# Optimization experiments

Hardware: AMD Instinct MI355X
Metric: run time of the kernel (lower is better)

## Reference

```python
import jax, jax.numpy as jnp
import numpy as np

IN_CH = 64
OUT_CH = 32
SCALE = 2
BLOCK = SCALE ** 3  # 8
N = 400000   # input sparse voxels (lines in pair_fwd)
M = 200000   # output sparse voxels


def setup_inputs() -> dict:
    key = jax.random.key(0)
    k1, k2, k3 = jax.random.split(key, 3)
    x_features = jax.random.normal(k1, (N, IN_CH), dtype=jnp.float32)
    # flat ParameterList: weights[i*BLOCK + j] is the (in_channels,) weight for
    # output channel i, kernel position j
    weights = jax.random.normal(k2, (BLOCK * OUT_CH, IN_CH), dtype=jnp.float32)
    # spconv pair_fwd: [kernel_volume, num_lines], -1 marks invalid mapping
    pair_fwd = jax.random.randint(k3, (BLOCK, N), -1, M)
    return {"x_features": x_features, "weights": weights,
            "pair_fwd": pair_fwd, "num_out": M}


def reference(x_features, weights, pair_fwd, num_out):
    block, n = pair_fwd.shape
    out_ch = weights.shape[0] // block
    # W[o, j, c] == weights_list[o*block + j]
    W = weights.reshape(out_ch, block, -1)
    # sequential VoxelShuffle then .view(-1) per block is identity on each
    # voxel's in_channels feature vector, so:
    # vals[j, n, o] = dot(W[o, j, :], x_features[n, :])
    vals = jnp.einsum('nc,ojc->jno', x_features, W)  # [block, N, out_ch]
    idx = pair_fwd.reshape(-1)                       # [block*N]
    # route invalid (-1) entries to a dummy trailing row
    safe = jnp.where(idx >= 0, idx, num_out)
    buf = jnp.zeros((num_out + 1, out_ch), dtype=vals.dtype)
    # original uses assignment (set) semantics into out_features
    buf = buf.at[safe].set(vals.reshape(block * n, out_ch))
    return buf[:num_out]
```

## Files before the change

kernel.cpp:

```cpp
#include <hip/hip_runtime.h>

#define IN_CH  64
#define OUT_CH 32
#define BLOCK  8
#define ROWS   8


__global__ void k_prep(int4* __restrict__ argmax4, int n4, int* __restrict__ cur) {
    int i = blockIdx.x * 256 + threadIdx.x;
    if (i < 16) cur[i] = 0;
    if (i < n4) argmax4[i] = make_int4(-1, -1, -1, -1);
}

__global__ void k_scatter_range(const int* __restrict__ pair, int* __restrict__ argmax,
                                int N, int jhi, int jlo, int flip) {
    int n = blockIdx.x * 256 + threadIdx.x;
    if (n >= N) return;
    if (flip) n = N - 1 - n;
    for (int j = jhi; j >= jlo; --j) {
        int t = j * N + n;
        int m = pair[t];
        if (m >= 0 && argmax[m] < t)
            atomicMax(&argmax[m], t);
    }
}

__global__ void k_fill(const int* __restrict__ argmax, int* __restrict__ cur,
                       int* __restrict__ bm, int* __restrict__ bn, int M, int N) {
    __shared__ int h9[9];
    __shared__ int b9[9];
    if (threadIdx.x < 9) h9[threadIdx.x] = 0;
    __syncthreads();
    int m = blockIdx.x * 256 + threadIdx.x;
    int j = 9, n = 0, lo = 0;
    if (m < M) {
        int t = argmax[m];
        if (t >= 0) { j = (int)((unsigned)t / (unsigned)N); n = t - j * N; }
        else j = 8;
        lo = atomicAdd(&h9[j], 1);
    }
    __syncthreads();
    if (threadIdx.x < 9 && h9[threadIdx.x] > 0)
        b9[threadIdx.x] = atomicAdd(&cur[threadIdx.x], h9[threadIdx.x]);
    __syncthreads();
    if (m < M) {
        int pos = j * M + b9[j] + lo;
        bm[pos] = m;
        bn[pos] = n;
    }
}

__global__ __launch_bounds__(512, 4) void k_compute(
        const float* __restrict__ x, const float* __restrict__ w,
        const int* __restrict__ cnt, const int* __restrict__ bm,
        const int* __restrict__ bn, float* __restrict__ out, int M, int N) {
    __shared__ __align__(16) float Xl[8][2][ROWS * 64];

    const int lane = threadIdx.x & 63;
    const int o    = lane & 31;
    const int hh   = lane >> 5;
    const int wv   = threadIdx.x >> 6;

    int T = blockIdx.x * 8 + wv;
    int j = 0, nrows = 0;
    for (; j < 9; ++j) {
        int c  = cnt[j];
        int nt = (c + 63) >> 6;
        if (T < nt) { nrows = min(64, c - T * 64); break; }
        T -= nt;
    }
    if (j >= 9) return;
    int base = j * M + T * 64;

    int jw = (j < 8) ? j : 0;
    float4 wreg[8];
#pragma unroll
    for (int k = 0; k < 8; ++k)
        wreg[k] = *(const float4*)&w[(o * BLOCK + jw) * IN_CH + hh * 32 + k * 4];

    int mm = 0, nn = 0;
    if (lane < nrows) { mm = bm[base + lane]; nn = bn[base + lane]; }

    int ntiles = (nrows + ROWS - 1) / ROWS;
    float ld[ROWS];

#pragma unroll
    for (int r = 0; r < ROWS; ++r) {
        int n = __builtin_amdgcn_readlane(nn, r);
        ld[r] = x[(size_t)n * IN_CH + lane];
    }

    for (int tile = 0; tile < ntiles; ++tile) {
        float* buf = &Xl[wv][tile & 1][0];
#pragma unroll
        for (int r = 0; r < ROWS; ++r)
            buf[r * 64 + lane] = ld[r];

        if (tile + 1 < ntiles) {
            int nb = (tile + 1) * ROWS;
#pragma unroll
            for (int r = 0; r < ROWS; ++r) {
                int n = __builtin_amdgcn_readlane(nn, nb + r);
                ld[r] = x[(size_t)n * IN_CH + lane];
            }
        }

        asm volatile("s_waitcnt lgkmcnt(0)" ::: "memory");

#pragma unroll
        for (int r = 0; r < ROWS; r += 2) {
            int grow = tile * ROWS + r;
            float s01[2];
#pragma unroll
            for (int p = 0; p < 2; ++p) {
                const float4* xp = (const float4*)(buf + (r + p) * 64) + hh * 8;
                float ax = 0.f, ay = 0.f, az = 0.f, aw = 0.f;
#pragma unroll
                for (int k = 0; k < 8; ++k) {
                    float4 xv = xp[k];
                    ax = fmaf(wreg[k].x, xv.x, ax);
                    ay = fmaf(wreg[k].y, xv.y, ay);
                    az = fmaf(wreg[k].z, xv.z, az);
                    aw = fmaf(wreg[k].w, xv.w, aw);
                }
                float s = (ax + ay) + (az + aw);
                s += __shfl_xor(s, 32);
                s01[p] = s;
            }
            float sv   = hh ? s01[1] : s01[0];
            int   m0   = __builtin_amdgcn_readlane(mm, grow);
            int   m1   = __builtin_amdgcn_readlane(mm, grow + 1);
            int   mrow = hh ? m1 : m0;
            if (j == 8) sv = 0.f;
            int orow = grow + hh;
            if (orow < nrows)
                out[(size_t)mrow * OUT_CH + o] = sv;
        }
    }
}

extern "C" void kernel_launch(void* const* d_in, const int* in_sizes, int n_in,
                              void* d_out, int out_size, void* d_ws, size_t ws_size,
                              hipStream_t stream) {
    const float* x    = (const float*)d_in[0];
    const float* w    = (const float*)d_in[1];
    const int*   pair = (const int*)d_in[2];
    int N = in_sizes[0] / IN_CH;
    int M = out_size / OUT_CH;

    char* ws     = (char*)d_ws;
    int*  cur    = (int*)ws;
    int*  argmax = (int*)(ws + 256);
    int*  bm     = (int*)(ws + 256 + (size_t)M * 4);
    int*  bn     = (int*)(ws + 256 + (size_t)M * 4 + (size_t)9 * M * 4);

    int n4 = M / 4;
    k_prep<<<(n4 + 255) / 256, 256, 0, stream>>>((int4*)argmax, n4, cur);

    int gN = (N + 255) / 256;
    k_scatter_range<<<gN, 256, 0, stream>>>(pair, argmax, N, 7, 7, 1);
    k_scatter_range<<<gN, 256, 0, stream>>>(pair, argmax, N, 6, 0, 0);

    k_fill<<<(M + 255) / 256, 256, 0, stream>>>(argmax, cur, bm, bn, M, N);

    int maxtiles = (M + 63) / 64 + 8;
    int blocks   = (maxtiles + 7) / 8;
    k_compute<<<blocks, 512, 0, stream>>>(x, w, cur, bm, bn, (float*)d_out, M, N);
}
```

Measured before the change: 99.79 us.

## Compute gathered rows with bf16 MFMA instead of fp32 FMA via LDS

Replaces the per-lane fp32 dot-product loop, which staged rows through shared memory, with bf16 MFMA 16x16x32 instructions. Activations and weights are converted to bf16 in registers, and x rows are gathered straight from global memory without the LDS double buffer. Blocks shrink to 256 threads. This cuts ALU and LDS traffic but lowers precision to bf16 inputs, which risks tolerance failures.

```diff
diff --git a/kernel.cpp b/kernel.cpp
--- a/kernel.cpp
+++ b/kernel.cpp
@@ -3,7 +3,9 @@
 #define IN_CH  64
 #define OUT_CH 32
 #define BLOCK  8
-#define ROWS   8
+
+using short8 = __attribute__((ext_vector_type(8))) short;
+using f32x4v = __attribute__((ext_vector_type(4))) float;
 
 
 __global__ void k_prep(int4* __restrict__ argmax4, int n4, int* __restrict__ cur) {
@@ -50,18 +52,31 @@
     }
 }
 
-__global__ __launch_bounds__(512, 4) void k_compute(
+__device__ __forceinline__ unsigned cvt_pk_bf16(float lo, float hi) {
+    unsigned r;
+    asm("v_cvt_pk_bf16_f32 %0, %1, %2" : "=v"(r) : "v"(lo), "v"(hi));
+    return r;
+}
+
+__device__ __forceinline__ short8 pack8(float4 a, float4 b) {
+    union { unsigned u[4]; short8 s; } p;
+    p.u[0] = cvt_pk_bf16(a.x, a.y);
+    p.u[1] = cvt_pk_bf16(a.z, a.w);
+    p.u[2] = cvt_pk_bf16(b.x, b.y);
+    p.u[3] = cvt_pk_bf16(b.z, b.w);
+    return p.s;
+}
+
+__global__ __launch_bounds__(256, 4) void k_compute(
         const float* __restrict__ x, const float* __restrict__ w,
         const int* __restrict__ cnt, const int* __restrict__ bm,
         const int* __restrict__ bn, float* __restrict__ out, int M, int N) {
-    __shared__ __align__(16) float Xl[8][2][ROWS * 64];
-
     const int lane = threadIdx.x & 63;
-    const int o    = lane & 31;
-    const int hh   = lane >> 5;
+    const int r16  = lane & 15;
+    const int kc   = lane >> 4;
     const int wv   = threadIdx.x >> 6;
 
-    int T = blockIdx.x * 8 + wv;
+    int T = blockIdx.x * 4 + wv;
     int j = 0, nrows = 0;
     for (; j < 9; ++j) {
         int c  = cnt[j];
@@ -71,70 +86,49 @@
     }
     if (j >= 9) return;
     int base = j * M + T * 64;
+    int jw = (j < 8) ? j : 0;
 
-    int jw = (j < 8) ? j : 0;
-    float4 wreg[8];
+    short8 bf[2][2];
 #pragma unroll
-    for (int k = 0; k < 8; ++k)
-        wreg[k] = *(const float4*)&w[(o * BLOCK + jw) * IN_CH + hh * 32 + k * 4];
-
-    int mm = 0, nn = 0;
-    if (lane < nrows) { mm = bm[base + lane]; nn = bn[base + lane]; }
-
-    int ntiles = (nrows + ROWS - 1) / ROWS;
-    float ld[ROWS];
+    for (int ot = 0; ot < 2; ++ot)
+#pragma unroll
+        for (int kk = 0; kk < 2; ++kk) {
+            const float* wp = w + ((ot * 16 + r16) * BLOCK + jw) * IN_CH + kk * 32 + kc * 8;
+            bf[ot][kk] = pack8(*(const float4*)wp, *(const float4*)(wp + 4));
+        }
 
 #pragma unroll
-    for (int r = 0; r < ROWS; ++r) {
-        int n = __builtin_amdgcn_readlane(nn, r);
-        ld[r] = x[(size_t)n * IN_CH + lane];
-    }
+    for (int st = 0; st < 4; ++st) {
+        if (st * 16 >= nrows) break;
+        int lrow = st * 16 + r16;
+        int n    = bn[base + ((lrow < nrows) ? lrow : 0)];
+        const float* xp = x + (size_t)n * IN_CH + kc * 8;
+        float4 x0 = *(const float4*)xp;
+        float4 x1 = *(const float4*)(xp + 4);
+        float4 x2 = *(const float4*)(xp + 32);
+        float4 x3 = *(const float4*)(xp + 36);
+        short8 a0 = pack8(x0, x1);
+        short8 a1 = pack8(x2, x3);
 
-    for (int tile = 0; tile < ntiles; ++tile) {
-        float* buf = &Xl[wv][tile & 1][0];
+        f32x4v acc0 = {0.f, 0.f, 0.f, 0.f};
+        f32x4v acc1 = {0.f, 0.f, 0.f, 0.f};
+        acc0 = __builtin_amdgcn_mfma_f32_16x16x32_bf16(a0, bf[0][0], acc0, 0, 0, 0);
+        acc0 = __builtin_amdgcn_mfma_f32_16x16x32_bf16(a1, bf[0][1], acc0, 0, 0, 0);
+        acc1 = __builtin_amdgcn_mfma_f32_16x16x32_bf16(a0, bf[1][0], acc1, 0, 0, 0);
+        acc1 = __builtin_amdgcn_mfma_f32_16x16x32_bf16(a1, bf[1][1], acc1, 0, 0, 0);
+
+        int4 m4 = *(const int4*)&bm[base + st * 16 + kc * 4];
+        int ma[4] = {m4.x, m4.y, m4.z, m4.w};
 #pragma unroll
-        for (int r = 0; r < ROWS; ++r)
-            buf[r * 64 + lane] = ld[r];
-
-        if (tile + 1 < ntiles) {
-            int nb = (tile + 1) * ROWS;
-#pragma unroll
-            for (int r = 0; r < ROWS; ++r) {
-                int n = __builtin_amdgcn_readlane(nn, nb + r);
-                ld[r] = x[(size_t)n * IN_CH + lane];
+        for (int q = 0; q < 4; ++q) {
+            int grow = st * 16 + kc * 4 + q;
+            if (grow < nrows) {
+                size_t ro = (size_t)ma[q] * OUT_CH;
+                float v0 = (j == 8) ? 0.f : acc0[q];
+                float v1 = (j == 8) ? 0.f : acc1[q];
+                out[ro + r16]      = v0;
+                out[ro + 16 + r16] = v1;
             }
-        }
-
-        asm volatile("s_waitcnt lgkmcnt(0)" ::: "memory");
-
-#pragma unroll
-        for (int r = 0; r < ROWS; r += 2) {
-            int grow = tile * ROWS + r;
-            float s01[2];
-#pragma unroll
-            for (int p = 0; p < 2; ++p) {
-                const float4* xp = (const float4*)(buf + (r + p) * 64) + hh * 8;
-                float ax = 0.f, ay = 0.f, az = 0.f, aw = 0.f;
-#pragma unroll
-                for (int k = 0; k < 8; ++k) {
-                    float4 xv = xp[k];
-                    ax = fmaf(wreg[k].x, xv.x, ax);
-                    ay = fmaf(wreg[k].y, xv.y, ay);
-                    az = fmaf(wreg[k].z, xv.z, az);
-                    aw = fmaf(wreg[k].w, xv.w, aw);
-                }
-                float s = (ax + ay) + (az + aw);
-                s += __shfl_xor(s, 32);
-                s01[p] = s;
-            }
-            float sv   = hh ? s01[1] : s01[0];
-            int   m0   = __builtin_amdgcn_readlane(mm, grow);
-            int   m1   = __builtin_amdgcn_readlane(mm, grow + 1);
-            int   mrow = hh ? m1 : m0;
-            if (j == 8) sv = 0.f;
-            int orow = grow + hh;
-            if (orow < nrows)
-                out[(size_t)mrow * OUT_CH + o] = sv;
         }
     }
 }
@@ -163,7 +157,7 @@
 
     k_fill<<<(M + 255) / 256, 256, 0, stream>>>(argmax, cur, bm, bn, M, N);
 
-    int maxtiles = (M + 63) / 64 + 8;
-    int blocks   = (maxtiles + 7) / 8;
-    k_compute<<<blocks, 512, 0, stream>>>(x, w, cur, bm, bn, (float*)d_out, M, N);
+    int maxtiles = (M + 63) / 64 + 9;
+    int blocks   = (maxtiles + 3) / 4;
+    k_compute<<<blocks, 256, 0, stream>>>(x, w, cur, bm, bn, (float*)d_out, M, N);
 }
```

Measured after the change: 91.30 us. 8.5% less time.
